# Optimization experiments

Hardware: AMD Instinct MI355X
Metric: run time of the kernel (lower is better)

The kernel has to match this reference:

```python
import jax, jax.numpy as jnp
import numpy as np

EPS = 1e-5


def setup_inputs() -> dict:
    key = jax.random.key(0)
    ks = jax.random.split(key, 8)
    b, n, l, e = 2, 16, 1024, 512
    qd, kd, vd = 64, 64, 64
    x = jax.random.normal(ks[0], (b, n, l, e), dtype=jnp.float32)
    past_kv = jax.random.normal(ks[1], (b, n, kd, vd), dtype=jnp.float32)
    s = 1.0 / np.sqrt(e)
    Wq = jax.random.normal(ks[2], (qd, e), dtype=jnp.float32) * s
    bq = jnp.zeros((qd,), dtype=jnp.float32)
    Wk = jax.random.normal(ks[3], (kd, e), dtype=jnp.float32) * s
    bk = jnp.zeros((kd,), dtype=jnp.float32)
    Wv = jax.random.normal(ks[4], (vd, e), dtype=jnp.float32) * s
    bv = jnp.zeros((vd,), dtype=jnp.float32)
    return {"x": x, "past_kv": past_kv, "Wq": Wq, "bq": bq,
            "Wk": Wk, "bk": bk, "Wv": Wv, "bv": bv}


def reference(x, past_kv, Wq, bq, Wk, bk, Wv, bv):
    b, n, l, e = x.shape
    # QKV projections on the last axis: [b,n,l,e] -> [b,n,l,d]
    q = jnp.einsum('bnle,de->bnld', x, Wq) + bq
    k = jnp.einsum('bnle,de->bnld', x, Wk) + bk
    v = jnp.einsum('bnle,de->bnld', x, Wv) + bv
    # RetNet per-head decay: 1 - 2^(-5-h), shape [1,n,1,1,1]
    decay = 1.0 - jnp.exp2(-5.0 - jnp.arange(n, dtype=jnp.float32))
    decay = decay.reshape(1, n, 1, 1, 1)
    # decayed state + per-position outer product k_t (x) v_t -> [b,n,l,kd,vd]
    current_kv = decay * past_kv[:, :, None, :, :] + k[..., :, None] * v[..., None, :]
    # Q-weighted reduction over k_dim -> [b,n,l,vd]
    out = jnp.einsum('bnlk,bnlkv->bnlv', q, current_kv)
    # F.group_norm(out, num_groups=n): per (b, head), normalize over (l, vd)
    mean = jnp.mean(out, axis=(2, 3), keepdims=True)
    var = jnp.var(out, axis=(2, 3), keepdims=True)
    out = (out - mean) * jax.lax.rsqrt(var + EPS)
    return out, current_kv
```

## Files before the change

kernel.cpp:

```cpp
#include <hip/hip_runtime.h>


constexpr int B  = 2;
constexpr int NH = 16;
constexpr int L  = 1024;
constexpr int E  = 512;
constexpr int D  = 64;
constexpr int M  = B * NH * L;
constexpr int NQKV = 192;
constexpr int BLK = 32;
constexpr int NBLKS = M / BLK;
constexpr float EPS = 1e-5f;

using short8 = __attribute__((ext_vector_type(8))) short;
using f32x4  = __attribute__((ext_vector_type(4))) float;

__device__ __forceinline__ unsigned short f2bf(float f) {
    union { float f; unsigned int u; } x; x.f = f;
    unsigned int u = x.u;
    return (unsigned short)((u + 0x7fffu + ((u >> 16) & 1u)) >> 16);
}
__device__ __forceinline__ float bf2f(unsigned short h) {
    union { unsigned int u; float f; } x; x.u = ((unsigned int)h) << 16;
    return x.f;
}

__global__ __launch_bounds__(256) void convw_kernel(
    const float* __restrict__ Wq, const float* __restrict__ Wk,
    const float* __restrict__ Wv, unsigned short* __restrict__ Wb)
{
    int idx = blockIdx.x * 256 + threadIdx.x;
    const float* src = (idx < 8192) ? Wq : (idx < 16384) ? Wk : Wv;
    int off = idx & 8191;
    float4 v = ((const float4*)src)[off];
    Wb[(size_t)idx * 4 + 0] = f2bf(v.x);
    Wb[(size_t)idx * 4 + 1] = f2bf(v.y);
    Wb[(size_t)idx * 4 + 2] = f2bf(v.z);
    Wb[(size_t)idx * 4 + 3] = f2bf(v.w);
}

__global__ __launch_bounds__(512) void proj_mfma_kernel(
    const float* __restrict__ x, const unsigned short* __restrict__ Wb,
    const float* __restrict__ bq, const float* __restrict__ bk,
    const float* __restrict__ bv,
    unsigned short* __restrict__ qkvb)
{
    constexpr int BM = 128, BK = 64, LDP = 72;
    __shared__ unsigned short Xs[BM][LDP];
    __shared__ unsigned short Ws[NQKV][LDP];
    __shared__ float bias_s[NQKV];

    const int tid  = threadIdx.x;
    const int row0 = blockIdx.x * BM;
    if (tid < NQKV)
        bias_s[tid] = (tid < 64) ? bq[tid] : (tid < 128) ? bk[tid - 64] : bv[tid - 128];

    const int wid  = tid >> 6;
    const int lane = tid & 63;
    const int wr   = wid >> 2;
    const int wc   = wid & 3;
    const int l15  = lane & 15;
    const int lk   = (lane >> 4) * 8;

    const int xr = tid >> 2;
    const int xc = (tid & 3) * 16;

    f32x4 acc[4][3] = {};

    for (int k0 = 0; k0 < E; k0 += BK) {
        float4 xa[4];
        #pragma unroll
        for (int i = 0; i < 4; ++i)
            xa[i] = *(const float4*)&x[(size_t)(row0 + xr) * E + k0 + xc + i * 4];
        short8 wch[3];
        #pragma unroll
        for (int i = 0; i < 3; ++i) {
            int c = tid + i * 512;
            wch[i] = *(const short8*)&Wb[(size_t)(c >> 3) * E + k0 + (c & 7) * 8];
        }
        __syncthreads();
        unsigned short tmp[16];
        #pragma unroll
        for (int i = 0; i < 4; ++i) {
            tmp[i*4+0] = f2bf(xa[i].x); tmp[i*4+1] = f2bf(xa[i].y);
            tmp[i*4+2] = f2bf(xa[i].z); tmp[i*4+3] = f2bf(xa[i].w);
        }
        *(short8*)&Xs[xr][xc]     = *(short8*)&tmp[0];
        *(short8*)&Xs[xr][xc + 8] = *(short8*)&tmp[8];
        #pragma unroll
        for (int i = 0; i < 3; ++i) {
            int c = tid + i * 512;
            *(short8*)&Ws[c >> 3][(c & 7) * 8] = wch[i];
        }
        __syncthreads();

        #pragma unroll
        for (int kk = 0; kk < 2; ++kk) {
            short8 a[4], b[3];
            #pragma unroll
            for (int mi = 0; mi < 4; ++mi)
                a[mi] = *(const short8*)&Xs[wr * 64 + mi * 16 + l15][kk * 32 + lk];
            #pragma unroll
            for (int ni = 0; ni < 3; ++ni)
                b[ni] = *(const short8*)&Ws[wc * 48 + ni * 16 + l15][kk * 32 + lk];
            #pragma unroll
            for (int mi = 0; mi < 4; ++mi)
                #pragma unroll
                for (int ni = 0; ni < 3; ++ni)
                    acc[mi][ni] = __builtin_amdgcn_mfma_f32_16x16x32_bf16(
                        a[mi], b[ni], acc[mi][ni], 0, 0, 0);
        }
    }

    #pragma unroll
    for (int mi = 0; mi < 4; ++mi) {
        #pragma unroll
        for (int ni = 0; ni < 3; ++ni) {
            int col = wc * 48 + ni * 16 + l15;
            float bb = bias_s[col];
            #pragma unroll
            for (int j = 0; j < 4; ++j) {
                int row = wr * 64 + mi * 16 + (lane >> 4) * 4 + j;
                qkvb[(size_t)(row0 + row) * NQKV + col] = f2bf(acc[mi][ni][j] + bb);
            }
        }
    }
}

__global__ __launch_bounds__(512) void retention_kernel(
    const unsigned short* __restrict__ qkvb,
    const float* __restrict__ past_kv,
    float* __restrict__ out_pre,
    float* __restrict__ ckv,
    float* __restrict__ partials)
{
    const int blk  = blockIdx.x;
    const int bn   = blk >> 5;
    const int pos0 = (blk & 31) * BLK;
    const int h    = bn & (NH - 1);
    const int tid  = threadIdx.x;
    const float decay = 1.0f - exp2f(-5.0f - (float)h);

    __shared__ float pkv_s[64 * 64];
    __shared__ unsigned short qkv_s[BLK * NQKV];
    __shared__ float qk_s[BLK];
    __shared__ float red[16];

    const float* pkv = past_kv + (size_t)bn * 4096;
    float4 p4[2];
    #pragma unroll
    for (int j = 0; j < 2; ++j) {
        p4[j] = *(const float4*)&pkv[(tid + j * 512) * 4];
        *(float4*)&pkv_s[(tid + j * 512) * 4] = p4[j];
    }
    const unsigned short* qrow = qkvb + (size_t)(bn * L + pos0) * NQKV;
    for (int f = tid; f < 768; f += 512)
        ((uint4*)qkv_s)[f] = ((const uint4*)qrow)[f];
    __syncthreads();

    {
        int pos = tid >> 4, c = tid & 15;
        const unsigned short* qp = &qkv_s[pos * NQKV];
        float p = 0.0f;
        #pragma unroll
        for (int j = 0; j < 4; ++j)
            p = fmaf(bf2f(qp[c * 4 + j]), bf2f(qp[64 + c * 4 + j]), p);
        p += __shfl_xor(p, 1); p += __shfl_xor(p, 2);
        p += __shfl_xor(p, 4); p += __shfl_xor(p, 8);
        if (c == 0) qk_s[pos] = p;
    }

    float* co = ckv + (size_t)(bn * L + pos0) * 4096;
    for (int pos = 0; pos < BLK; ++pos) {
        const unsigned short* ks = &qkv_s[pos * NQKV + 64];
        const unsigned short* vs = &qkv_s[pos * NQKV + 128];
        #pragma unroll
        for (int j = 0; j < 2; ++j) {
            int f = tid + j * 512;
            float kk = bf2f(ks[f >> 4]);
            const unsigned short* vp = &vs[(f & 15) * 4];
            float4 r;
            r.x = fmaf(decay, p4[j].x, kk * bf2f(vp[0]));
            r.y = fmaf(decay, p4[j].y, kk * bf2f(vp[1]));
            r.z = fmaf(decay, p4[j].z, kk * bf2f(vp[2]));
            r.w = fmaf(decay, p4[j].w, kk * bf2f(vp[3]));
            *(float4*)&co[(size_t)pos * 4096 + f * 4] = r;
        }
    }
    __syncthreads();

    const int wave = tid >> 6, lane = tid & 63;
    const int vd = lane;
    float accs[4] = {0.0f, 0.0f, 0.0f, 0.0f};
    for (int kd = 0; kd < 64; ++kd) {
        float pv = pkv_s[kd * 64 + vd];
        #pragma unroll
        for (int pp = 0; pp < 4; ++pp)
            accs[pp] = fmaf(bf2f(qkv_s[(wave + pp * 8) * NQKV + kd]), pv, accs[pp]);
    }
    float s1 = 0.0f, s2 = 0.0f;
    #pragma unroll
    for (int pp = 0; pp < 4; ++pp) {
        int pos = wave + pp * 8;
        float o = fmaf(decay, accs[pp],
                       qk_s[pos] * bf2f(qkv_s[pos * NQKV + 128 + vd]));
        out_pre[(size_t)(bn * L + pos0 + pos) * D + vd] = o;
        s1 += o; s2 += o * o;
    }

    #pragma unroll
    for (int off = 32; off; off >>= 1) {
        s1 += __shfl_down(s1, off);
        s2 += __shfl_down(s2, off);
    }
    if (lane == 0) { red[wave * 2] = s1; red[wave * 2 + 1] = s2; }
    __syncthreads();
    if (tid == 0) {
        float a = 0.0f, b2 = 0.0f;
        #pragma unroll
        for (int w = 0; w < 8; ++w) { a += red[w * 2]; b2 += red[w * 2 + 1]; }
        partials[(size_t)blk * 2]     = a;
        partials[(size_t)blk * 2 + 1] = b2;
    }
}

__global__ __launch_bounds__(64) void group_reduce_kernel(
    const float* __restrict__ partials, float* __restrict__ stats)
{
    const int g   = blockIdx.x;
    const int tid = threadIdx.x;
    float s1 = 0.0f, s2 = 0.0f;
    if (tid < 32) {
        s1 = partials[(size_t)(g * 32 + tid) * 2];
        s2 = partials[(size_t)(g * 32 + tid) * 2 + 1];
    }
    #pragma unroll
    for (int off = 16; off; off >>= 1) {
        s1 += __shfl_down(s1, off);
        s2 += __shfl_down(s2, off);
    }
    if (tid == 0) {
        const float cnt = (float)(L * D);
        float mean = s1 / cnt;
        float var  = s2 / cnt - mean * mean;
        stats[g * 2]     = mean;
        stats[g * 2 + 1] = rsqrtf(var + EPS);
    }
}

__global__ __launch_bounds__(256) void normalize_kernel(
    float* __restrict__ out, const float* __restrict__ stats)
{
    int idx = blockIdx.x * 256 + threadIdx.x;
    int g = idx >> 14;
    float mean = stats[g * 2];
    float rstd = stats[g * 2 + 1];
    float4 v = ((const float4*)out)[idx];
    v.x = (v.x - mean) * rstd; v.y = (v.y - mean) * rstd;
    v.z = (v.z - mean) * rstd; v.w = (v.w - mean) * rstd;
    ((float4*)out)[idx] = v;
}

extern "C" void kernel_launch(void* const* d_in, const int* in_sizes, int n_in,
                              void* d_out, int out_size, void* d_ws, size_t ws_size,
                              hipStream_t stream)
{
    const float* x       = (const float*)d_in[0];
    const float* past_kv = (const float*)d_in[1];
    const float* Wq      = (const float*)d_in[2];
    const float* bq      = (const float*)d_in[3];
    const float* Wk      = (const float*)d_in[4];
    const float* bk      = (const float*)d_in[5];
    const float* Wv      = (const float*)d_in[6];
    const float* bv      = (const float*)d_in[7];

    float* out = (float*)d_out;
    float* ckv = out + (size_t)M * 64;

    unsigned short* Wb   = (unsigned short*)d_ws;
    unsigned short* qkvb = Wb + (size_t)NQKV * E;
    float* partials = (float*)(qkvb + (size_t)M * NQKV);
    float* stats    = partials + (size_t)NBLKS * 2;

    convw_kernel<<<96, 256, 0, stream>>>(Wq, Wk, Wv, Wb);
    proj_mfma_kernel<<<M / 128, 512, 0, stream>>>(x, Wb, bq, bk, bv, qkvb);
    retention_kernel<<<NBLKS, 512, 0, stream>>>(qkvb, past_kv, out, ckv, partials);
    group_reduce_kernel<<<32, 64, 0, stream>>>(partials, stats);
    normalize_kernel<<<(M * 16) / 256, 256, 0, stream>>>(out, stats);
}
```

Before: 139.7 us.

## Fuse QKV projection into retention kernel, keeping QKV tile in shared memory

Merges the MFMA projection kernel and the retention kernel into one kernel. Each 256-thread block computes a 64-row QKV tile and writes it to reused shared memory, then builds the decayed KV outer products and the output from that tile. This removes the bf16 QKV round trip through global memory and one kernel launch. In exchange each block handles 64 positions with fewer threads and a smaller MFMA tile, and the large ckv write stays the dominant cost.

```diff
diff --git a/kernel.cpp b/kernel.cpp
--- a/kernel.cpp
+++ b/kernel.cpp
@@ -8,7 +8,7 @@
 constexpr int D  = 64;
 constexpr int M  = B * NH * L;
 constexpr int NQKV = 192;
-constexpr int BLK = 32;
+constexpr int BLK = 64;
 constexpr int NBLKS = M / BLK;
 constexpr float EPS = 1e-5f;
 
@@ -39,58 +39,74 @@
     Wb[(size_t)idx * 4 + 3] = f2bf(v.w);
 }
 
-__global__ __launch_bounds__(512) void proj_mfma_kernel(
-    const float* __restrict__ x, const unsigned short* __restrict__ Wb,
+__global__ __launch_bounds__(256) void fused_kernel(
+    const float* __restrict__ x,
+    const unsigned short* __restrict__ Wb,
     const float* __restrict__ bq, const float* __restrict__ bk,
     const float* __restrict__ bv,
-    unsigned short* __restrict__ qkvb)
-{
-    constexpr int BM = 128, BK = 64, LDP = 72;
-    __shared__ unsigned short Xs[BM][LDP];
-    __shared__ unsigned short Ws[NQKV][LDP];
-    __shared__ float bias_s[NQKV];
-
+    const float* __restrict__ past_kv,
+    float* __restrict__ out_pre,
+    float* __restrict__ ckv,
+    float* __restrict__ partials)
+{
+    constexpr int LDP = 72;
+    constexpr int QSP = 200;
+    __shared__ __align__(16) unsigned char smem[(64 * LDP + 192 * LDP) * 2];
+    auto Xs = (unsigned short(*)[LDP])smem;
+    auto Ws = (unsigned short(*)[LDP])(smem + 64 * LDP * 2);
+    auto qs = (unsigned short(*)[QSP])smem;
+    __shared__ float pkv_s[64 * 64];
+    __shared__ float qk_s[BLK];
+    __shared__ float red[8];
+
+    const int blk  = blockIdx.x;
+    const int bn   = blk >> 4;
+    const int pos0 = (blk & 15) * BLK;
+    const int h    = bn & (NH - 1);
     const int tid  = threadIdx.x;
-    const int row0 = blockIdx.x * BM;
-    if (tid < NQKV)
-        bias_s[tid] = (tid < 64) ? bq[tid] : (tid < 128) ? bk[tid - 64] : bv[tid - 128];
+    const float decay = 1.0f - exp2f(-5.0f - (float)h);
+
+    const float* pkv = past_kv + (size_t)bn * 4096;
+    float4 p4[4];
+    #pragma unroll
+    for (int j = 0; j < 4; ++j) {
+        p4[j] = *(const float4*)&pkv[(tid + j * 256) * 4];
+        *(float4*)&pkv_s[(tid + j * 256) * 4] = p4[j];
+    }
 
     const int wid  = tid >> 6;
     const int lane = tid & 63;
-    const int wr   = wid >> 2;
-    const int wc   = wid & 3;
     const int l15  = lane & 15;
     const int lk   = (lane >> 4) * 8;
 
-    const int xr = tid >> 2;
-    const int xc = (tid & 3) * 16;
-
+    const float* xrow = x + (size_t)(bn * L + pos0) * E;
     f32x4 acc[4][3] = {};
 
-    for (int k0 = 0; k0 < E; k0 += BK) {
+    for (int k0 = 0; k0 < E; k0 += 64) {
         float4 xa[4];
         #pragma unroll
-        for (int i = 0; i < 4; ++i)
-            xa[i] = *(const float4*)&x[(size_t)(row0 + xr) * E + k0 + xc + i * 4];
-        short8 wch[3];
-        #pragma unroll
-        for (int i = 0; i < 3; ++i) {
-            int c = tid + i * 512;
-            wch[i] = *(const short8*)&Wb[(size_t)(c >> 3) * E + k0 + (c & 7) * 8];
+        for (int j = 0; j < 4; ++j) {
+            int f = tid + j * 256;
+            xa[j] = *(const float4*)&xrow[(size_t)(f >> 4) * E + k0 + (f & 15) * 4];
+        }
+        short8 wch[6];
+        #pragma unroll
+        for (int j = 0; j < 6; ++j) {
+            int c = tid + j * 256;
+            wch[j] = *(const short8*)&Wb[(size_t)(c >> 3) * E + k0 + (c & 7) * 8];
         }
         __syncthreads();
-        unsigned short tmp[16];
-        #pragma unroll
-        for (int i = 0; i < 4; ++i) {
-            tmp[i*4+0] = f2bf(xa[i].x); tmp[i*4+1] = f2bf(xa[i].y);
-            tmp[i*4+2] = f2bf(xa[i].z); tmp[i*4+3] = f2bf(xa[i].w);
-        }
-        *(short8*)&Xs[xr][xc]     = *(short8*)&tmp[0];
-        *(short8*)&Xs[xr][xc + 8] = *(short8*)&tmp[8];
-        #pragma unroll
-        for (int i = 0; i < 3; ++i) {
-            int c = tid + i * 512;
-            *(short8*)&Ws[c >> 3][(c & 7) * 8] = wch[i];
+        #pragma unroll
+        for (int j = 0; j < 4; ++j) {
+            int f = tid + j * 256;
+            unsigned short t4[4] = {f2bf(xa[j].x), f2bf(xa[j].y),
+                                    f2bf(xa[j].z), f2bf(xa[j].w)};
+            *(uint2*)&Xs[f >> 4][(f & 15) * 4] = *(uint2*)t4;
+        }
+        #pragma unroll
+        for (int j = 0; j < 6; ++j) {
+            int c = tid + j * 256;
+            *(short8*)&Ws[c >> 3][(c & 7) * 8] = wch[j];
         }
         __syncthreads();
 
@@ -99,10 +115,10 @@
             short8 a[4], b[3];
             #pragma unroll
             for (int mi = 0; mi < 4; ++mi)
-                a[mi] = *(const short8*)&Xs[wr * 64 + mi * 16 + l15][kk * 32 + lk];
+                a[mi] = *(const short8*)&Xs[mi * 16 + l15][kk * 32 + lk];
             #pragma unroll
             for (int ni = 0; ni < 3; ++ni)
-                b[ni] = *(const short8*)&Ws[wc * 48 + ni * 16 + l15][kk * 32 + lk];
+                b[ni] = *(const short8*)&Ws[wid * 48 + ni * 16 + l15][kk * 32 + lk];
             #pragma unroll
             for (int mi = 0; mi < 4; ++mi)
                 #pragma unroll
@@ -111,72 +127,43 @@
                         a[mi], b[ni], acc[mi][ni], 0, 0, 0);
         }
     }
-
-    #pragma unroll
-    for (int mi = 0; mi < 4; ++mi) {
-        #pragma unroll
-        for (int ni = 0; ni < 3; ++ni) {
-            int col = wc * 48 + ni * 16 + l15;
-            float bb = bias_s[col];
+    __syncthreads();
+
+    #pragma unroll
+    for (int ni = 0; ni < 3; ++ni) {
+        int col = wid * 48 + ni * 16 + l15;
+        float bb = (col < 64) ? bq[col] : (col < 128) ? bk[col - 64] : bv[col - 128];
+        #pragma unroll
+        for (int mi = 0; mi < 4; ++mi) {
             #pragma unroll
             for (int j = 0; j < 4; ++j) {
-                int row = wr * 64 + mi * 16 + (lane >> 4) * 4 + j;
-                qkvb[(size_t)(row0 + row) * NQKV + col] = f2bf(acc[mi][ni][j] + bb);
+                int row = mi * 16 + (lane >> 4) * 4 + j;
+                qs[row][col] = f2bf(acc[mi][ni][j] + bb);
             }
         }
     }
-}
-
-__global__ __launch_bounds__(512) void retention_kernel(
-    const unsigned short* __restrict__ qkvb,
-    const float* __restrict__ past_kv,
-    float* __restrict__ out_pre,
-    float* __restrict__ ckv,
-    float* __restrict__ partials)
-{
-    const int blk  = blockIdx.x;
-    const int bn   = blk >> 5;
-    const int pos0 = (blk & 31) * BLK;
-    const int h    = bn & (NH - 1);
-    const int tid  = threadIdx.x;
-    const float decay = 1.0f - exp2f(-5.0f - (float)h);
-
-    __shared__ float pkv_s[64 * 64];
-    __shared__ unsigned short qkv_s[BLK * NQKV];
-    __shared__ float qk_s[BLK];
-    __shared__ float red[16];
-
-    const float* pkv = past_kv + (size_t)bn * 4096;
-    float4 p4[2];
-    #pragma unroll
-    for (int j = 0; j < 2; ++j) {
-        p4[j] = *(const float4*)&pkv[(tid + j * 512) * 4];
-        *(float4*)&pkv_s[(tid + j * 512) * 4] = p4[j];
-    }
-    const unsigned short* qrow = qkvb + (size_t)(bn * L + pos0) * NQKV;
-    for (int f = tid; f < 768; f += 512)
-        ((uint4*)qkv_s)[f] = ((const uint4*)qrow)[f];
     __syncthreads();
 
     {
-        int pos = tid >> 4, c = tid & 15;
-        const unsigned short* qp = &qkv_s[pos * NQKV];
+        int pos = tid >> 2, c = tid & 3;
         float p = 0.0f;
         #pragma unroll
-        for (int j = 0; j < 4; ++j)
-            p = fmaf(bf2f(qp[c * 4 + j]), bf2f(qp[64 + c * 4 + j]), p);
+        for (int j = 0; j < 16; ++j) {
+            int e = c * 16 + j;
+            p = fmaf(bf2f(qs[pos][e]), bf2f(qs[pos][64 + e]), p);
+        }
         p += __shfl_xor(p, 1); p += __shfl_xor(p, 2);
-        p += __shfl_xor(p, 4); p += __shfl_xor(p, 8);
         if (c == 0) qk_s[pos] = p;
     }
+    __syncthreads();
 
     float* co = ckv + (size_t)(bn * L + pos0) * 4096;
     for (int pos = 0; pos < BLK; ++pos) {
-        const unsigned short* ks = &qkv_s[pos * NQKV + 64];
-        const unsigned short* vs = &qkv_s[pos * NQKV + 128];
-        #pragma unroll
-        for (int j = 0; j < 2; ++j) {
-            int f = tid + j * 512;
+        const unsigned short* ks = &qs[pos][64];
+        const unsigned short* vs = &qs[pos][128];
+        #pragma unroll
+        for (int j = 0; j < 4; ++j) {
+            int f = tid + j * 256;
             float kk = bf2f(ks[f >> 4]);
             const unsigned short* vp = &vs[(f & 15) * 4];
             float4 r;
@@ -187,23 +174,20 @@
             *(float4*)&co[(size_t)pos * 4096 + f * 4] = r;
         }
     }
-    __syncthreads();
-
-    const int wave = tid >> 6, lane = tid & 63;
+
     const int vd = lane;
-    float accs[4] = {0.0f, 0.0f, 0.0f, 0.0f};
+    float accs[16] = {};
     for (int kd = 0; kd < 64; ++kd) {
         float pv = pkv_s[kd * 64 + vd];
         #pragma unroll
-        for (int pp = 0; pp < 4; ++pp)
-            accs[pp] = fmaf(bf2f(qkv_s[(wave + pp * 8) * NQKV + kd]), pv, accs[pp]);
+        for (int pp = 0; pp < 16; ++pp)
+            accs[pp] = fmaf(bf2f(qs[wid + pp * 4][kd]), pv, accs[pp]);
     }
     float s1 = 0.0f, s2 = 0.0f;
     #pragma unroll
-    for (int pp = 0; pp < 4; ++pp) {
-        int pos = wave + pp * 8;
-        float o = fmaf(decay, accs[pp],
-                       qk_s[pos] * bf2f(qkv_s[pos * NQKV + 128 + vd]));
+    for (int pp = 0; pp < 16; ++pp) {
+        int pos = wid + pp * 4;
+        float o = fmaf(decay, accs[pp], qk_s[pos] * bf2f(qs[pos][128 + vd]));
         out_pre[(size_t)(bn * L + pos0 + pos) * D + vd] = o;
         s1 += o; s2 += o * o;
     }
@@ -213,12 +197,12 @@
         s1 += __shfl_down(s1, off);
         s2 += __shfl_down(s2, off);
     }
-    if (lane == 0) { red[wave * 2] = s1; red[wave * 2 + 1] = s2; }
+    if (lane == 0) { red[wid * 2] = s1; red[wid * 2 + 1] = s2; }
     __syncthreads();
     if (tid == 0) {
         float a = 0.0f, b2 = 0.0f;
         #pragma unroll
-        for (int w = 0; w < 8; ++w) { a += red[w * 2]; b2 += red[w * 2 + 1]; }
+        for (int w = 0; w < 4; ++w) { a += red[w * 2]; b2 += red[w * 2 + 1]; }
         partials[(size_t)blk * 2]     = a;
         partials[(size_t)blk * 2 + 1] = b2;
     }
@@ -230,12 +214,12 @@
     const int g   = blockIdx.x;
     const int tid = threadIdx.x;
     float s1 = 0.0f, s2 = 0.0f;
-    if (tid < 32) {
-        s1 = partials[(size_t)(g * 32 + tid) * 2];
-        s2 = partials[(size_t)(g * 32 + tid) * 2 + 1];
-    }
-    #pragma unroll
-    for (int off = 16; off; off >>= 1) {
+    if (tid < 16) {
+        s1 = partials[(size_t)(g * 16 + tid) * 2];
+        s2 = partials[(size_t)(g * 16 + tid) * 2 + 1];
+    }
+    #pragma unroll
+    for (int off = 8; off; off >>= 1) {
         s1 += __shfl_down(s1, off);
         s2 += __shfl_down(s2, off);
     }
@@ -277,14 +261,13 @@
     float* out = (float*)d_out;
     float* ckv = out + (size_t)M * 64;
 
-    unsigned short* Wb   = (unsigned short*)d_ws;
-    unsigned short* qkvb = Wb + (size_t)NQKV * E;
-    float* partials = (float*)(qkvb + (size_t)M * NQKV);
+    unsigned short* Wb = (unsigned short*)d_ws;
+    float* partials = (float*)(Wb + (size_t)NQKV * E);
     float* stats    = partials + (size_t)NBLKS * 2;
 
     convw_kernel<<<96, 256, 0, stream>>>(Wq, Wk, Wv, Wb);
-    proj_mfma_kernel<<<M / 128, 512, 0, stream>>>(x, Wb, bq, bk, bv, qkvb);
-    retention_kernel<<<NBLKS, 512, 0, stream>>>(qkvb, past_kv, out, ckv, partials);
+    fused_kernel<<<NBLKS, 256, 0, stream>>>(x, Wb, bq, bk, bv, past_kv,
+                                            out, ckv, partials);
     group_reduce_kernel<<<32, 64, 0, stream>>>(partials, stats);
     normalize_kernel<<<(M * 16) / 256, 256, 0, stream>>>(out, stats);
 }
```

After: 206.0 us. +47.5%, slower.
